# Kernel optimization log

Measured on AMD Instinct MI355X. Metric: run time of the kernel, lower is better.

Reference implementation:

```python
import jax, jax.numpy as jnp
import numpy as np


def setup_inputs() -> dict:
    key = jax.random.key(0)
    ks = jax.random.split(key, 6)
    B, Q, K = 4, 512, 1024
    Dq, Dk, Dv, H = 512, 512, 512, 128
    return {
        "queries": jax.random.normal(ks[0], (B, Q, Dq), dtype=jnp.float32),
        "keys": jax.random.normal(ks[1], (B, K, Dk), dtype=jnp.float32),
        "values": jax.random.normal(ks[2], (B, K, Dv), dtype=jnp.float32),
        "W_q": jax.random.normal(ks[3], (Dq, H), dtype=jnp.float32) / np.sqrt(Dq),
        "W_k": jax.random.normal(ks[4], (Dk, H), dtype=jnp.float32) / np.sqrt(Dk),
        "w_v": jax.random.normal(ks[5], (H,), dtype=jnp.float32) / np.sqrt(H),
    }


def reference(queries, keys, values, W_q, W_k, w_v):
    # Additive (Bahdanau) attention.
    q = jnp.einsum("bqd,dh->bqh", queries, W_q)          # [B,Q,H]
    k = jnp.einsum("bkd,dh->bkh", keys, W_k)             # [B,K,H]
    features = jnp.tanh(q[:, :, None, :] + k[:, None, :, :])  # [B,Q,K,H]
    scores = jnp.einsum("bqkh,h->bqk", features, w_v)    # [B,Q,K]
    attn = jax.nn.softmax(scores, axis=-1)               # [B,Q,K]
    return jnp.einsum("bqk,bkv->bqv", attn, values)      # [B,Q,Dv]
```

## Files before the change

kernel.cpp:

```cpp
#include <hip/hip_runtime.h>

#define BB   4
#define QS   512
#define KSZ  1024
#define DD   512
#define HH   128
#define DVV  512

typedef unsigned int uint;
typedef unsigned short ushort;
typedef unsigned long long ull;
typedef __attribute__((ext_vector_type(8)))  short short8;
typedef __attribute__((ext_vector_type(16))) float f32x16;

__device__ __forceinline__ float rcp_fast(float x)  { return __builtin_amdgcn_rcpf(x); }
__device__ __forceinline__ float exp2_fast(float x) { return __builtin_amdgcn_exp2f(x); }

__device__ __forceinline__ void split1(float v, ushort& h, ushort& l) {
    uint u = __float_as_uint(v);
    h = (ushort)(u >> 16);
    float r = v - __uint_as_float(u & 0xffff0000u);
    l = (ushort)(__float_as_uint(r) >> 16);
}

#define NSQ  (BB * QS * DD / 4 / 256)
#define NSK  (BB * KSZ * DD / 4 / 256)
#define NWT  128
#define NPJ  192
#define NVT  (BB * (KSZ / 32) * (DVV / 32))

__global__ __launch_bounds__(256) void split_kernel(
    const float* __restrict__ q, const float* __restrict__ k,
    const float* __restrict__ Wq, const float* __restrict__ Wk,
    ushort* __restrict__ qh, ushort* __restrict__ ql,
    ushort* __restrict__ kh, ushort* __restrict__ kl,
    ushort* __restrict__ wqh, ushort* __restrict__ wql,
    ushort* __restrict__ wkh, ushort* __restrict__ wkl)
{
    const int id  = blockIdx.x;
    const int tid = threadIdx.x;

    if (id < NSQ + NSK) {
        const float* src; ushort* dh; ushort* dl; size_t i;
        if (id < NSQ) { src = q; dh = qh; dl = ql; i = (size_t)id * 256 + tid; }
        else          { src = k; dh = kh; dl = kl; i = (size_t)(id - NSQ) * 256 + tid; }
        float4 v = ((const float4*)src)[i];
        ushort h0,h1,h2,h3,l0,l1,l2,l3;
        split1(v.x,h0,l0); split1(v.y,h1,l1); split1(v.z,h2,l2); split1(v.w,h3,l3);
        *(ushort4*)&dh[i * 4] = make_ushort4(h0,h1,h2,h3);
        *(ushort4*)&dl[i * 4] = make_ushort4(l0,l1,l2,l3);
        return;
    }
    __shared__ float Ts[32][33];
    int t = id - (NSQ + NSK);
    const float* W; ushort* dh; ushort* dl;
    if (t < 64) { W = Wq; dh = wqh; dl = wql; }
    else        { W = Wk; dh = wkh; dl = wkl; t -= 64; }
    const int d0 = (t >> 2) * 32, h0 = (t & 3) * 32;
    {
        const int dd = tid >> 3, c4 = (tid & 7) * 4;
        float4 v = *(const float4*)&W[(size_t)(d0 + dd) * HH + h0 + c4];
        Ts[dd][c4 + 0] = v.x; Ts[dd][c4 + 1] = v.y;
        Ts[dd][c4 + 2] = v.z; Ts[dd][c4 + 3] = v.w;
    }
    __syncthreads();
    {
        const int hh = tid >> 3, d4 = (tid & 7) * 4;
        ushort h[4], l[4];
        #pragma unroll
        for (int i = 0; i < 4; i++) split1(Ts[d4 + i][hh], h[i], l[i]);
        size_t o = (size_t)(h0 + hh) * DD + d0 + d4;
        *(ushort4*)&dh[o] = make_ushort4(h[0], h[1], h[2], h[3]);
        *(ushort4*)&dl[o] = make_ushort4(l[0], l[1], l[2], l[3]);
    }
}

__global__ __launch_bounds__(256) void projvt_kernel(
    const ushort* __restrict__ qh, const ushort* __restrict__ ql,
    const ushort* __restrict__ kh, const ushort* __restrict__ kl,
    const ushort* __restrict__ wqh, const ushort* __restrict__ wql,
    const ushort* __restrict__ wkh, const ushort* __restrict__ wkl,
    const float* __restrict__ val,
    float* __restrict__ eq, float* __restrict__ ek,
    ushort* __restrict__ vhi, ushort* __restrict__ vlo)
{
    const int id  = blockIdx.x;
    const int tid = threadIdx.x;

    if (id >= NPJ) {
        __shared__ float Ts[32][33];
        const int t   = id - NPJ;
        const int b   = t >> 9;
        const int rem = t & 511;
        const int k0  = (rem >> 4) * 32;
        const int n0  = (rem & 15) * 32;
        {
            const int kk = tid >> 3, n4 = (tid & 7) * 4;
            float4 v = *(const float4*)&val[((size_t)b * KSZ + k0 + kk) * DVV + n0 + n4];
            Ts[kk][n4 + 0] = v.x; Ts[kk][n4 + 1] = v.y;
            Ts[kk][n4 + 2] = v.z; Ts[kk][n4 + 3] = v.w;
        }
        __syncthreads();
        {
            const int nn = tid >> 3, k4 = (tid & 7) * 4;
            ushort h[4], l[4];
            #pragma unroll
            for (int i = 0; i < 4; i++) split1(Ts[k4 + i][nn], h[i], l[i]);
            size_t o = ((size_t)b * DVV + n0 + nn) * KSZ + k0 + k4;
            *(ushort4*)&vhi[o] = make_ushort4(h[0], h[1], h[2], h[3]);
            *(ushort4*)&vlo[o] = make_ushort4(l[0], l[1], l[2], l[3]);
        }
        return;
    }

    const int w = tid >> 6, lane = tid & 63;
    const int row = lane & 31, kg = lane >> 5;
    const int gw = id * 4 + w;

    const ushort *pa_h, *pa_l, *pb_h, *pb_l; float* op; int m0, nt;
    if (gw < 256) {
        m0 = (gw >> 2) * 32; nt = gw & 3;
        pa_h = qh; pa_l = ql; pb_h = wqh; pb_l = wql; op = eq;
    } else {
        const int g = gw - 256;
        m0 = (g >> 2) * 32; nt = g & 3;
        pa_h = kh; pa_l = kl; pb_h = wkh; pb_l = wkl; op = ek;
    }

    const ushort* ah_p = pa_h + (size_t)(m0 + row) * DD + kg * 8;
    const ushort* al_p = pa_l + (size_t)(m0 + row) * DD + kg * 8;
    const ushort* bh_p = pb_h + (size_t)(nt * 32 + row) * DD + kg * 8;
    const ushort* bl_p = pb_l + (size_t)(nt * 32 + row) * DD + kg * 8;

    f32x16 acc;
    #pragma unroll
    for (int i = 0; i < 16; i++) acc[i] = 0.f;

    #pragma unroll 8
    for (int ks = 0; ks < DD; ks += 16) {
        short8 ah = *(const short8*)(ah_p + ks);
        short8 al = *(const short8*)(al_p + ks);
        short8 bh = *(const short8*)(bh_p + ks);
        short8 bl = *(const short8*)(bl_p + ks);
        acc = __builtin_amdgcn_mfma_f32_32x32x16_bf16(ah, bh, acc, 0, 0, 0);
        acc = __builtin_amdgcn_mfma_f32_32x32x16_bf16(ah, bl, acc, 0, 0, 0);
        acc = __builtin_amdgcn_mfma_f32_32x32x16_bf16(al, bh, acc, 0, 0, 0);
    }

    const float C2L = 2.8853900817779268f;
    float* ob = op + (size_t)m0 * HH + nt * 32;
    #pragma unroll
    for (int r = 0; r < 16; r++) {
        const int rb = (r & 3) + 8 * (r >> 2) + 4 * kg;
        ob[(size_t)rb * HH + row] = exp2_fast(acc[r] * C2L);
    }
}

__global__ __launch_bounds__(512, 2) void spv_kernel(
    const float* __restrict__ eq, const float* __restrict__ ek,
    const float* __restrict__ wv,
    const ushort* __restrict__ vhi, const ushort* __restrict__ vlo,
    float* __restrict__ opart, float* __restrict__ rsp)
{
    __shared__ float  eqs[64][132];
    __shared__ float  eks[32][132];
    __shared__ ushort PhS[64][36];
    __shared__ ushort PlS[64][36];

    const int id  = blockIdx.x;
    const int bk  = id & 31;
    const int qt  = id >> 5;
    const int b   = bk >> 3;
    const int kp  = bk & 7;

    const int tid  = threadIdx.x;
    const int w    = tid >> 6, lane = tid & 63;
    const int col  = lane & 31, kg = lane >> 5;
    const int wq   = (w & 1) * 32;
    const int wn   = (w >> 1) * 128;
    const int tq   = tid >> 4;
    const int tk   = tid & 15;

    const float* eqg = eq + ((size_t)b * QS + qt * 64) * HH;
    #pragma unroll
    for (int i = 0; i < 4; i++) {
        int f = tid + i * 512;
        int row = f >> 5, c4 = (f & 31) * 4;
        *(float4*)&eqs[row][c4] = *(const float4*)&eqg[(size_t)row * HH + c4];
    }
    const float* ekg = ek + ((size_t)b * KSZ + kp * 128) * HH;
    #pragma unroll
    for (int i = 0; i < 2; i++) {
        int f = tid + i * 512;
        int row = f >> 5, c4 = (f & 31) * 4;
        *(float4*)&eks[row][c4] = *(const float4*)&ekg[(size_t)row * HH + c4];
    }
    __syncthreads();

    f32x16 acc[4];
    #pragma unroll
    for (int n = 0; n < 4; n++) {
        #pragma unroll
        for (int i = 0; i < 16; i++) acc[n][i] = 0.f;
    }
    float rowacc0 = 0.f, rowacc1 = 0.f;

    const size_t vrow0 = ((size_t)b * DVV + wn + col) * KSZ + kp * 128;
    const ushort* vh_p = vhi + vrow0;
    const ushort* vl_p = vlo + vrow0;

#define SGROUP(eqv, ekv, sacc) { \
    float u0 = fminf(fmaf((eqv).x, (ekv).x, 1.0f), 3e7f); \
    float u1 = fminf(fmaf((eqv).y, (ekv).y, 1.0f), 3e7f); \
    float u2 = fminf(fmaf((eqv).z, (ekv).z, 1.0f), 3e7f); \
    float u3 = fminf(fmaf((eqv).w, (ekv).w, 1.0f), 3e7f); \
    float p01 = u0 * u1, p23 = u2 * u3; \
    float n01 = fmaf(wv4.x, u1, wv4.y * u0); \
    float n23 = fmaf(wv4.z, u3, wv4.w * u2); \
    float Nn = fmaf(n01, p23, n23 * p01); \
    sacc = fmaf(Nn, rcp_fast(p01 * p23), sacc); }

    for (int s = 0; s < 4; s++) {
        uint4 bhf[8], blf[8];
        #pragma unroll
        for (int nb = 0; nb < 4; nb++) {
            #pragma unroll
            for (int k2 = 0; k2 < 2; k2++) {
                const size_t o = (size_t)(nb * 32) * KSZ + s * 32 + k2 * 16 + kg * 8;
                bhf[nb * 2 + k2] = *(const uint4*)(vh_p + o);
                blf[nb * 2 + k2] = *(const uint4*)(vl_p + o);
            }
        }
        float4 eknxt0, eknxt1;
        if (s < 3) {
            int f0 = tid, f1 = tid + 512;
            eknxt0 = *(const float4*)&ekg[(size_t)((s + 1) * 32 + (f0 >> 5)) * HH + (f0 & 31) * 4];
            eknxt1 = *(const float4*)&ekg[(size_t)((s + 1) * 32 + (f1 >> 5)) * HH + (f1 & 31) * 4];
        }

        float s00 = 0.f, s01 = 0.f, s10 = 0.f, s11 = 0.f;
        #pragma unroll 2
        for (int h = 0; h < HH; h += 4) {
            float4 wv4 = *(const float4*)&wv[h];
            float4 eqa = *(const float4*)&eqs[tq][h];
            float4 eqb = *(const float4*)&eqs[tq + 32][h];
            float4 eka = *(const float4*)&eks[tk][h];
            float4 ekb = *(const float4*)&eks[tk + 16][h];
            SGROUP(eqa, eka, s00);
            SGROUP(eqa, ekb, s01);
            SGROUP(eqb, eka, s10);
            SGROUP(eqb, ekb, s11);
        }
        {
            const float CN = -2.8853900817779268f;
            float p00 = exp2_fast(s00 * CN);
            float p01v = exp2_fast(s01 * CN);
            float p10 = exp2_fast(s10 * CN);
            float p11 = exp2_fast(s11 * CN);
            ushort hh, ll;
            split1(p00,  hh, ll); PhS[tq][tk]           = hh; PlS[tq][tk]           = ll;
            split1(p01v, hh, ll); PhS[tq][tk + 16]      = hh; PlS[tq][tk + 16]      = ll;
            split1(p10,  hh, ll); PhS[tq + 32][tk]      = hh; PlS[tq + 32][tk]      = ll;
            split1(p11,  hh, ll); PhS[tq + 32][tk + 16] = hh; PlS[tq + 32][tk + 16] = ll;
            rowacc0 += p00 + p01v;
            rowacc1 += p10 + p11;
        }
        __syncthreads();

        if (s < 3) {
            int f0 = tid, f1 = tid + 512;
            *(float4*)&eks[f0 >> 5][(f0 & 31) * 4] = eknxt0;
            *(float4*)&eks[f1 >> 5][(f1 & 31) * 4] = eknxt1;
        }

        #pragma unroll
        for (int k2 = 0; k2 < 2; k2++) {
            short8 ah, al;
            { const ull* p = (const ull*)&PhS[wq + col][k2 * 16 + kg * 8];
              ((ull*)&ah)[0] = p[0]; ((ull*)&ah)[1] = p[1]; }
            { const ull* p = (const ull*)&PlS[wq + col][k2 * 16 + kg * 8];
              ((ull*)&al)[0] = p[0]; ((ull*)&al)[1] = p[1]; }
            #pragma unroll
            for (int nb = 0; nb < 4; nb++) {
                short8 vh = *(const short8*)&bhf[nb * 2 + k2];
                short8 vl = *(const short8*)&blf[nb * 2 + k2];
                acc[nb] = __builtin_amdgcn_mfma_f32_32x32x16_bf16(ah, vh, acc[nb], 0, 0, 0);
                acc[nb] = __builtin_amdgcn_mfma_f32_32x32x16_bf16(ah, vl, acc[nb], 0, 0, 0);
                acc[nb] = __builtin_amdgcn_mfma_f32_32x32x16_bf16(al, vh, acc[nb], 0, 0, 0);
            }
        }
        __syncthreads();
    }
#undef SGROUP

    #pragma unroll
    for (int m = 8; m; m >>= 1) {
        rowacc0 += __shfl_xor(rowacc0, m);
        rowacc1 += __shfl_xor(rowacc1, m);
    }
    if (tk == 0) {
        rsp[((size_t)b * QS + qt * 64 + tq) * 8 + kp]      = rowacc0;
        rsp[((size_t)b * QS + qt * 64 + tq + 32) * 8 + kp] = rowacc1;
    }

    float* ob = opart + (((size_t)kp * BB + b) * QS + qt * 64 + wq) * DVV + wn;
    #pragma unroll
    for (int nb = 0; nb < 4; nb++) {
        #pragma unroll
        for (int r = 0; r < 16; r++) {
            const int rb = (r & 3) + 8 * (r >> 2) + 4 * kg;
            ob[(size_t)rb * DVV + nb * 32 + col] = acc[nb][r];
        }
    }
}

__global__ __launch_bounds__(256) void norm_kernel(
    const float* __restrict__ opart, const float* __restrict__ rsp,
    float* __restrict__ outp)
{
    const int i  = blockIdx.x * 256 + threadIdx.x;
    const int n4 = (i & 127) * 4;
    const int q  = (i >> 7) & (QS - 1);
    const int b  = i >> 16;

    const float* rp = rsp + ((size_t)b * QS + q) * 8;
    float4 r0 = *(const float4*)rp;
    float4 r1 = *(const float4*)(rp + 4);
    float inv = rcp_fast(r0.x + r0.y + r0.z + r0.w + r1.x + r1.y + r1.z + r1.w);

    float ox = 0.f, oy = 0.f, oz = 0.f, ow = 0.f;
    #pragma unroll
    for (int kp = 0; kp < 8; kp++) {
        float4 v = *(const float4*)&opart[(((size_t)kp * BB + b) * QS + q) * DVV + n4];
        ox += v.x; oy += v.y; oz += v.z; ow += v.w;
    }
    float4 res = make_float4(ox * inv, oy * inv, oz * inv, ow * inv);
    *(float4*)&outp[((size_t)b * QS + q) * DVV + n4] = res;
}

extern "C" void kernel_launch(void* const* d_in, const int* in_sizes, int n_in,
                              void* d_out, int out_size, void* d_ws, size_t ws_size,
                              hipStream_t stream)
{
    const float* queries = (const float*)d_in[0];
    const float* keys    = (const float*)d_in[1];
    const float* values  = (const float*)d_in[2];
    const float* Wq      = (const float*)d_in[3];
    const float* Wk      = (const float*)d_in[4];
    const float* wv      = (const float*)d_in[5];
    float* out = (float*)d_out;

    float*  eq    = (float*)d_ws;
    float*  ek    = eq  + (size_t)BB * QS * HH;
    float*  rsp   = ek  + (size_t)BB * KSZ * HH;
    float*  opart = rsp + (size_t)BB * QS * 8;
    ushort* vhi = (ushort*)(opart + (size_t)8 * BB * QS * DVV);
    ushort* vlo = vhi + (size_t)BB * KSZ * DVV;
    ushort* qh  = vlo + (size_t)BB * KSZ * DVV;
    ushort* ql  = qh  + (size_t)BB * QS * DD;
    ushort* kh  = ql  + (size_t)BB * QS * DD;
    ushort* kl  = kh  + (size_t)BB * KSZ * DD;
    ushort* wqh = kl  + (size_t)BB * KSZ * DD;
    ushort* wql = wqh + (size_t)HH * DD;
    ushort* wkh = wql + (size_t)HH * DD;
    ushort* wkl = wkh + (size_t)HH * DD;

    split_kernel<<<dim3(NSQ + NSK + NWT), 256, 0, stream>>>(
        queries, keys, Wq, Wk, qh, ql, kh, kl, wqh, wql, wkh, wkl);

    projvt_kernel<<<dim3(NPJ + NVT), 256, 0, stream>>>(
        qh, ql, kh, kl, wqh, wql, wkh, wkl, values, eq, ek, vhi, vlo);

    spv_kernel<<<dim3(256), 512, 0, stream>>>(eq, ek, wv, vhi, vlo, opart, rsp);

    norm_kernel<<<dim3(1024), 256, 0, stream>>>(opart, rsp, out);
}
```

Baseline: 152.3 us.

## Retile score-PV kernel into 16-query blocks with 16x16x32 MFMA

The fused score+PV kernel now processes 16 queries per 256-thread block instead of 64 queries per 512-thread block, launching 1024 blocks instead of 256 to fill the CUs better. The PV matmul switches from 32x32x16 to 16x16x32 bf16 MFMA with 8 accumulator tiles per wave, and each wave covers 128 output columns. The block index mapping is reordered so neighbouring blocks share the batch/key slice. The cost is that V tiles are re-read by four times as many blocks, and each block has less reuse of its staged ek tile.

```diff
diff --git a/kernel.cpp b/kernel.cpp
--- a/kernel.cpp
+++ b/kernel.cpp
@@ -12,6 +12,7 @@
 typedef unsigned long long ull;
 typedef __attribute__((ext_vector_type(8)))  short short8;
 typedef __attribute__((ext_vector_type(16))) float f32x16;
+typedef __attribute__((ext_vector_type(4)))  float f32x4;
 
 __device__ __forceinline__ float rcp_fast(float x)  { return __builtin_amdgcn_rcpf(x); }
 __device__ __forceinline__ float exp2_fast(float x) { return __builtin_amdgcn_exp2f(x); }
@@ -156,58 +157,60 @@
     }
 }
 
-__global__ __launch_bounds__(512, 2) void spv_kernel(
+__global__ __launch_bounds__(256, 4) void spv_kernel(
     const float* __restrict__ eq, const float* __restrict__ ek,
     const float* __restrict__ wv,
     const ushort* __restrict__ vhi, const ushort* __restrict__ vlo,
     float* __restrict__ opart, float* __restrict__ rsp)
 {
-    __shared__ float  eqs[64][132];
+    __shared__ float  eqs[16][132];
     __shared__ float  eks[32][132];
-    __shared__ ushort PhS[64][36];
-    __shared__ ushort PlS[64][36];
-
-    const int id  = blockIdx.x;
-    const int bk  = id & 31;
-    const int qt  = id >> 5;
-    const int b   = bk >> 3;
-    const int kp  = bk & 7;
+    __shared__ ushort PhS[16][36];
+    __shared__ ushort PlS[16][36];
+
+    const int id   = blockIdx.x;
+    const int low3 = id & 7;
+    const int rest = id >> 3;
+    const int bk   = (rest & 3) * 8 + low3;
+    const int qt   = rest >> 2;
+    const int b    = bk >> 3;
+    const int kp   = bk & 7;
 
     const int tid  = threadIdx.x;
     const int w    = tid >> 6, lane = tid & 63;
-    const int col  = lane & 31, kg = lane >> 5;
-    const int wq   = (w & 1) * 32;
-    const int wn   = (w >> 1) * 128;
     const int tq   = tid >> 4;
     const int tk   = tid & 15;
-
-    const float* eqg = eq + ((size_t)b * QS + qt * 64) * HH;
+    const int wn   = w * 128;
+    const int arow = lane & 15;
+    const int akg  = lane >> 4;
+
+    const float* eqg = eq + ((size_t)b * QS + qt * 16) * HH;
+    #pragma unroll
+    for (int i = 0; i < 2; i++) {
+        int f = tid + i * 256;
+        *(float4*)&eqs[f >> 5][(f & 31) * 4] =
+            *(const float4*)&eqg[(size_t)(f >> 5) * HH + (f & 31) * 4];
+    }
+    const float* ekg = ek + ((size_t)b * KSZ + kp * 128) * HH;
     #pragma unroll
     for (int i = 0; i < 4; i++) {
-        int f = tid + i * 512;
-        int row = f >> 5, c4 = (f & 31) * 4;
-        *(float4*)&eqs[row][c4] = *(const float4*)&eqg[(size_t)row * HH + c4];
-    }
-    const float* ekg = ek + ((size_t)b * KSZ + kp * 128) * HH;
-    #pragma unroll
-    for (int i = 0; i < 2; i++) {
-        int f = tid + i * 512;
-        int row = f >> 5, c4 = (f & 31) * 4;
-        *(float4*)&eks[row][c4] = *(const float4*)&ekg[(size_t)row * HH + c4];
+        int f = tid + i * 256;
+        *(float4*)&eks[f >> 5][(f & 31) * 4] =
+            *(const float4*)&ekg[(size_t)(f >> 5) * HH + (f & 31) * 4];
     }
     __syncthreads();
 
-    f32x16 acc[4];
-    #pragma unroll
-    for (int n = 0; n < 4; n++) {
+    f32x4 acc[8];
+    #pragma unroll
+    for (int n = 0; n < 8; n++) {
         #pragma unroll
-        for (int i = 0; i < 16; i++) acc[n][i] = 0.f;
-    }
-    float rowacc0 = 0.f, rowacc1 = 0.f;
-
-    const size_t vrow0 = ((size_t)b * DVV + wn + col) * KSZ + kp * 128;
-    const ushort* vh_p = vhi + vrow0;
-    const ushort* vl_p = vlo + vrow0;
+        for (int i = 0; i < 4; i++) acc[n][i] = 0.f;
+    }
+    float rowacc = 0.f;
+
+    const size_t vrow0 = ((size_t)b * DVV + wn + arow) * KSZ + kp * 128 + akg * 8;
+    const ushort* vhb = vhi + vrow0;
+    const ushort* vlb = vlo + vrow0;
 
 #define SGROUP(eqv, ekv, sacc) { \
     float u0 = fminf(fmaf((eqv).x, (ekv).x, 1.0f), 3e7f); \
@@ -221,96 +224,75 @@
     sacc = fmaf(Nn, rcp_fast(p01 * p23), sacc); }
 
     for (int s = 0; s < 4; s++) {
-        uint4 bhf[8], blf[8];
-        #pragma unroll
-        for (int nb = 0; nb < 4; nb++) {
+        float4 eknxt[4];
+        if (s < 3) {
             #pragma unroll
-            for (int k2 = 0; k2 < 2; k2++) {
-                const size_t o = (size_t)(nb * 32) * KSZ + s * 32 + k2 * 16 + kg * 8;
-                bhf[nb * 2 + k2] = *(const uint4*)(vh_p + o);
-                blf[nb * 2 + k2] = *(const uint4*)(vl_p + o);
+            for (int i = 0; i < 4; i++) {
+                int f = tid + i * 256;
+                eknxt[i] = *(const float4*)
+                    &ekg[(size_t)((s + 1) * 32 + (f >> 5)) * HH + (f & 31) * 4];
             }
         }
-        float4 eknxt0, eknxt1;
-        if (s < 3) {
-            int f0 = tid, f1 = tid + 512;
-            eknxt0 = *(const float4*)&ekg[(size_t)((s + 1) * 32 + (f0 >> 5)) * HH + (f0 & 31) * 4];
-            eknxt1 = *(const float4*)&ekg[(size_t)((s + 1) * 32 + (f1 >> 5)) * HH + (f1 & 31) * 4];
-        }
-
-        float s00 = 0.f, s01 = 0.f, s10 = 0.f, s11 = 0.f;
-        #pragma unroll 2
+
+        float s0 = 0.f, s1 = 0.f;
+        #pragma unroll 4
         for (int h = 0; h < HH; h += 4) {
             float4 wv4 = *(const float4*)&wv[h];
             float4 eqa = *(const float4*)&eqs[tq][h];
-            float4 eqb = *(const float4*)&eqs[tq + 32][h];
             float4 eka = *(const float4*)&eks[tk][h];
             float4 ekb = *(const float4*)&eks[tk + 16][h];
-            SGROUP(eqa, eka, s00);
-            SGROUP(eqa, ekb, s01);
-            SGROUP(eqb, eka, s10);
-            SGROUP(eqb, ekb, s11);
+            SGROUP(eqa, eka, s0);
+            SGROUP(eqa, ekb, s1);
         }
         {
             const float CN = -2.8853900817779268f;
-            float p00 = exp2_fast(s00 * CN);
-            float p01v = exp2_fast(s01 * CN);
-            float p10 = exp2_fast(s10 * CN);
-            float p11 = exp2_fast(s11 * CN);
+            float p0 = exp2_fast(s0 * CN);
+            float p1 = exp2_fast(s1 * CN);
             ushort hh, ll;
-            split1(p00,  hh, ll); PhS[tq][tk]           = hh; PlS[tq][tk]           = ll;
-            split1(p01v, hh, ll); PhS[tq][tk + 16]      = hh; PlS[tq][tk + 16]      = ll;
-            split1(p10,  hh, ll); PhS[tq + 32][tk]      = hh; PlS[tq + 32][tk]      = ll;
-            split1(p11,  hh, ll); PhS[tq + 32][tk + 16] = hh; PlS[tq + 32][tk + 16] = ll;
-            rowacc0 += p00 + p01v;
-            rowacc1 += p10 + p11;
+            split1(p0, hh, ll); PhS[tq][tk]      = hh; PlS[tq][tk]      = ll;
+            split1(p1, hh, ll); PhS[tq][tk + 16] = hh; PlS[tq][tk + 16] = ll;
+            rowacc += p0 + p1;
         }
         __syncthreads();
 
         if (s < 3) {
-            int f0 = tid, f1 = tid + 512;
-            *(float4*)&eks[f0 >> 5][(f0 & 31) * 4] = eknxt0;
-            *(float4*)&eks[f1 >> 5][(f1 & 31) * 4] = eknxt1;
-        }
-
+            #pragma unroll
+            for (int i = 0; i < 4; i++) {
+                int f = tid + i * 256;
+                *(float4*)&eks[f >> 5][(f & 31) * 4] = eknxt[i];
+            }
+        }
+
+        short8 ah, al;
+        { const ull* p = (const ull*)&PhS[arow][akg * 8];
+          ((ull*)&ah)[0] = p[0]; ((ull*)&ah)[1] = p[1]; }
+        { const ull* p = (const ull*)&PlS[arow][akg * 8];
+          ((ull*)&al)[0] = p[0]; ((ull*)&al)[1] = p[1]; }
         #pragma unroll
-        for (int k2 = 0; k2 < 2; k2++) {
-            short8 ah, al;
-            { const ull* p = (const ull*)&PhS[wq + col][k2 * 16 + kg * 8];
-              ((ull*)&ah)[0] = p[0]; ((ull*)&ah)[1] = p[1]; }
-            { const ull* p = (const ull*)&PlS[wq + col][k2 * 16 + kg * 8];
-              ((ull*)&al)[0] = p[0]; ((ull*)&al)[1] = p[1]; }
-            #pragma unroll
-            for (int nb = 0; nb < 4; nb++) {
-                short8 vh = *(const short8*)&bhf[nb * 2 + k2];
-                short8 vl = *(const short8*)&blf[nb * 2 + k2];
-                acc[nb] = __builtin_amdgcn_mfma_f32_32x32x16_bf16(ah, vh, acc[nb], 0, 0, 0);
-                acc[nb] = __builtin_amdgcn_mfma_f32_32x32x16_bf16(ah, vl, acc[nb], 0, 0, 0);
-                acc[nb] = __builtin_amdgcn_mfma_f32_32x32x16_bf16(al, vh, acc[nb], 0, 0, 0);
-            }
+        for (int nb = 0; nb < 8; nb++) {
+            const size_t o = (size_t)nb * 16 * KSZ + (size_t)s * 32;
+            short8 vh = *(const short8*)(vhb + o);
+            short8 vl = *(const short8*)(vlb + o);
+            acc[nb] = __builtin_amdgcn_mfma_f32_16x16x32_bf16(ah, vh, acc[nb], 0, 0, 0);
+            acc[nb] = __builtin_amdgcn_mfma_f32_16x16x32_bf16(ah, vl, acc[nb], 0, 0, 0);
+            acc[nb] = __builtin_amdgcn_mfma_f32_16x16x32_bf16(al, vh, acc[nb], 0, 0, 0);
         }
         __syncthreads();
     }
 #undef SGROUP
 
     #pragma unroll
-    for (int m = 8; m; m >>= 1) {
-        rowacc0 += __shfl_xor(rowacc0, m);
-        rowacc1 += __shfl_xor(rowacc1, m);
-    }
-    if (tk == 0) {
-        rsp[((size_t)b * QS + qt * 64 + tq) * 8 + kp]      = rowacc0;
-        rsp[((size_t)b * QS + qt * 64 + tq + 32) * 8 + kp] = rowacc1;
-    }
-
-    float* ob = opart + (((size_t)kp * BB + b) * QS + qt * 64 + wq) * DVV + wn;
-    #pragma unroll
-    for (int nb = 0; nb < 4; nb++) {
+    for (int m = 8; m; m >>= 1) rowacc += __shfl_xor(rowacc, m);
+    if (tk == 0)
+        rsp[((size_t)b * QS + qt * 16 + tq) * 8 + kp] = rowacc;
+
+    float* ob = opart + (((size_t)kp * BB + b) * QS + qt * 16) * DVV + wn;
+    const int orow = akg * 4;
+    #pragma unroll
+    for (int nb = 0; nb < 8; nb++) {
         #pragma unroll
-        for (int r = 0; r < 16; r++) {
-            const int rb = (r & 3) + 8 * (r >> 2) + 4 * kg;
-            ob[(size_t)rb * DVV + nb * 32 + col] = acc[nb][r];
-        }
+        for (int r = 0; r < 4; r++)
+            ob[(size_t)(orow + r) * DVV + nb * 16 + arow] = acc[nb][r];
     }
 }
 
@@ -371,7 +353,7 @@
     projvt_kernel<<<dim3(NPJ + NVT), 256, 0, stream>>>(
         qh, ql, kh, kl, wqh, wql, wkh, wkl, values, eq, ek, vhi, vlo);
 
-    spv_kernel<<<dim3(256), 512, 0, stream>>>(eq, ek, wv, vhi, vlo, opart, rsp);
+    spv_kernel<<<dim3(1024), 256, 0, stream>>>(eq, ek, wv, vhi, vlo, opart, rsp);
 
     norm_kernel<<<dim3(1024), 256, 0, stream>>>(opart, rsp, out);
 }
```

After: 158.9 us. 4.3% more time.

## Split score-PV kernel into smaller 32x64 tiles with 16-way key partitioning

Applied to the files above, without the earlier changes.

Retiles the fused score/softmax-weighted-V kernel from 256 blocks of 512 threads (64 queries x 128 keys) to 1024 blocks of 256 threads (32 queries x 64 keys), doubling the key partitions to 16. This aims to fill more compute units on the MI355X and raise occupancy. The V-fragment prefetch and ek double-buffer prefetch are replaced with loads issued directly before the MFMAs, and the extra key partitions double the partial output buffer written and then reduced by the norm kernel.

```diff
diff --git a/kernel.cpp b/kernel.cpp
--- a/kernel.cpp
+++ b/kernel.cpp
@@ -6,6 +6,7 @@
 #define DD   512
 #define HH   128
 #define DVV  512
+#define KPN  16
 
 typedef unsigned int uint;
 typedef unsigned short ushort;
@@ -156,44 +157,43 @@
     }
 }
 
-__global__ __launch_bounds__(512, 2) void spv_kernel(
+__global__ __launch_bounds__(256, 4) void spv_kernel(
     const float* __restrict__ eq, const float* __restrict__ ek,
     const float* __restrict__ wv,
     const ushort* __restrict__ vhi, const ushort* __restrict__ vlo,
     float* __restrict__ opart, float* __restrict__ rsp)
 {
-    __shared__ float  eqs[64][132];
+    __shared__ float  eqs[32][132];
     __shared__ float  eks[32][132];
-    __shared__ ushort PhS[64][36];
-    __shared__ ushort PlS[64][36];
+    __shared__ ushort PhS[32][36];
+    __shared__ ushort PlS[32][36];
 
     const int id  = blockIdx.x;
-    const int bk  = id & 31;
-    const int qt  = id >> 5;
-    const int b   = bk >> 3;
-    const int kp  = bk & 7;
+    const int kp  = id & 15;
+    const int b   = (id >> 4) & 3;
+    const int qt  = id >> 6;
 
     const int tid  = threadIdx.x;
     const int w    = tid >> 6, lane = tid & 63;
-    const int col  = lane & 31, kg = lane >> 5;
-    const int wq   = (w & 1) * 32;
-    const int wn   = (w >> 1) * 128;
     const int tq   = tid >> 4;
     const int tk   = tid & 15;
-
-    const float* eqg = eq + ((size_t)b * QS + qt * 64) * HH;
+    const int wn   = w * 128;
+    const int arow = lane & 31;
+    const int akg  = lane >> 5;
+
+    const float* eqg = eq + ((size_t)b * QS + qt * 32) * HH;
     #pragma unroll
     for (int i = 0; i < 4; i++) {
-        int f = tid + i * 512;
-        int row = f >> 5, c4 = (f & 31) * 4;
-        *(float4*)&eqs[row][c4] = *(const float4*)&eqg[(size_t)row * HH + c4];
-    }
-    const float* ekg = ek + ((size_t)b * KSZ + kp * 128) * HH;
-    #pragma unroll
-    for (int i = 0; i < 2; i++) {
-        int f = tid + i * 512;
-        int row = f >> 5, c4 = (f & 31) * 4;
-        *(float4*)&eks[row][c4] = *(const float4*)&ekg[(size_t)row * HH + c4];
+        int f = tid + i * 256;
+        *(float4*)&eqs[f >> 5][(f & 31) * 4] =
+            *(const float4*)&eqg[(size_t)(f >> 5) * HH + (f & 31) * 4];
+    }
+    const float* ekg = ek + ((size_t)b * KSZ + kp * 64) * HH;
+    #pragma unroll
+    for (int i = 0; i < 4; i++) {
+        int f = tid + i * 256;
+        *(float4*)&eks[f >> 5][(f & 31) * 4] =
+            *(const float4*)&ekg[(size_t)(f >> 5) * HH + (f & 31) * 4];
     }
     __syncthreads();
 
@@ -205,9 +205,9 @@
     }
     float rowacc0 = 0.f, rowacc1 = 0.f;
 
-    const size_t vrow0 = ((size_t)b * DVV + wn + col) * KSZ + kp * 128;
-    const ushort* vh_p = vhi + vrow0;
-    const ushort* vl_p = vlo + vrow0;
+    const size_t vrow0 = ((size_t)b * DVV + wn + arow) * KSZ + kp * 64 + akg * 8;
+    const ushort* vhb = vhi + vrow0;
+    const ushort* vlb = vlo + vrow0;
 
 #define SGROUP(eqv, ekv, sacc) { \
     float u0 = fminf(fmaf((eqv).x, (ekv).x, 1.0f), 3e7f); \
@@ -220,30 +220,14 @@
     float Nn = fmaf(n01, p23, n23 * p01); \
     sacc = fmaf(Nn, rcp_fast(p01 * p23), sacc); }
 
-    for (int s = 0; s < 4; s++) {
-        uint4 bhf[8], blf[8];
-        #pragma unroll
-        for (int nb = 0; nb < 4; nb++) {
-            #pragma unroll
-            for (int k2 = 0; k2 < 2; k2++) {
-                const size_t o = (size_t)(nb * 32) * KSZ + s * 32 + k2 * 16 + kg * 8;
-                bhf[nb * 2 + k2] = *(const uint4*)(vh_p + o);
-                blf[nb * 2 + k2] = *(const uint4*)(vl_p + o);
-            }
-        }
-        float4 eknxt0, eknxt1;
-        if (s < 3) {
-            int f0 = tid, f1 = tid + 512;
-            eknxt0 = *(const float4*)&ekg[(size_t)((s + 1) * 32 + (f0 >> 5)) * HH + (f0 & 31) * 4];
-            eknxt1 = *(const float4*)&ekg[(size_t)((s + 1) * 32 + (f1 >> 5)) * HH + (f1 & 31) * 4];
-        }
-
+    #pragma unroll
+    for (int s = 0; s < 2; s++) {
         float s00 = 0.f, s01 = 0.f, s10 = 0.f, s11 = 0.f;
-        #pragma unroll 2
+        #pragma unroll 4
         for (int h = 0; h < HH; h += 4) {
             float4 wv4 = *(const float4*)&wv[h];
             float4 eqa = *(const float4*)&eqs[tq][h];
-            float4 eqb = *(const float4*)&eqs[tq + 32][h];
+            float4 eqb = *(const float4*)&eqs[tq + 16][h];
             float4 eka = *(const float4*)&eks[tk][h];
             float4 ekb = *(const float4*)&eks[tk + 16][h];
             SGROUP(eqa, eka, s00);
@@ -260,34 +244,44 @@
             ushort hh, ll;
             split1(p00,  hh, ll); PhS[tq][tk]           = hh; PlS[tq][tk]           = ll;
             split1(p01v, hh, ll); PhS[tq][tk + 16]      = hh; PlS[tq][tk + 16]      = ll;
-            split1(p10,  hh, ll); PhS[tq + 32][tk]      = hh; PlS[tq + 32][tk]      = ll;
-            split1(p11,  hh, ll); PhS[tq + 32][tk + 16] = hh; PlS[tq + 32][tk + 16] = ll;
+            split1(p10,  hh, ll); PhS[tq + 16][tk]      = hh; PlS[tq + 16][tk]      = ll;
+            split1(p11,  hh, ll); PhS[tq + 16][tk + 16] = hh; PlS[tq + 16][tk + 16] = ll;
             rowacc0 += p00 + p01v;
             rowacc1 += p10 + p11;
         }
         __syncthreads();
 
-        if (s < 3) {
-            int f0 = tid, f1 = tid + 512;
-            *(float4*)&eks[f0 >> 5][(f0 & 31) * 4] = eknxt0;
-            *(float4*)&eks[f1 >> 5][(f1 & 31) * 4] = eknxt1;
-        }
-
+        if (s == 0) {
+            #pragma unroll
+            for (int i = 0; i < 4; i++) {
+                int f = tid + i * 256;
+                *(float4*)&eks[f >> 5][(f & 31) * 4] =
+                    *(const float4*)&ekg[(size_t)(32 + (f >> 5)) * HH + (f & 31) * 4];
+            }
+        }
+
+        short8 ah0, al0, ah1, al1;
+        { const ull* p = (const ull*)&PhS[arow][akg * 8];
+          ((ull*)&ah0)[0] = p[0]; ((ull*)&ah0)[1] = p[1]; }
+        { const ull* p = (const ull*)&PlS[arow][akg * 8];
+          ((ull*)&al0)[0] = p[0]; ((ull*)&al0)[1] = p[1]; }
+        { const ull* p = (const ull*)&PhS[arow][16 + akg * 8];
+          ((ull*)&ah1)[0] = p[0]; ((ull*)&ah1)[1] = p[1]; }
+        { const ull* p = (const ull*)&PlS[arow][16 + akg * 8];
+          ((ull*)&al1)[0] = p[0]; ((ull*)&al1)[1] = p[1]; }
         #pragma unroll
-        for (int k2 = 0; k2 < 2; k2++) {
-            short8 ah, al;
-            { const ull* p = (const ull*)&PhS[wq + col][k2 * 16 + kg * 8];
-              ((ull*)&ah)[0] = p[0]; ((ull*)&ah)[1] = p[1]; }
-            { const ull* p = (const ull*)&PlS[wq + col][k2 * 16 + kg * 8];
-              ((ull*)&al)[0] = p[0]; ((ull*)&al)[1] = p[1]; }
-            #pragma unroll
-            for (int nb = 0; nb < 4; nb++) {
-                short8 vh = *(const short8*)&bhf[nb * 2 + k2];
-                short8 vl = *(const short8*)&blf[nb * 2 + k2];
-                acc[nb] = __builtin_amdgcn_mfma_f32_32x32x16_bf16(ah, vh, acc[nb], 0, 0, 0);
-                acc[nb] = __builtin_amdgcn_mfma_f32_32x32x16_bf16(ah, vl, acc[nb], 0, 0, 0);
-                acc[nb] = __builtin_amdgcn_mfma_f32_32x32x16_bf16(al, vh, acc[nb], 0, 0, 0);
-            }
+        for (int nb = 0; nb < 4; nb++) {
+            const size_t o = (size_t)nb * 32 * KSZ + (size_t)s * 32;
+            short8 vh0 = *(const short8*)(vhb + o);
+            short8 vl0 = *(const short8*)(vlb + o);
+            short8 vh1 = *(const short8*)(vhb + o + 16);
+            short8 vl1 = *(const short8*)(vlb + o + 16);
+            acc[nb] = __builtin_amdgcn_mfma_f32_32x32x16_bf16(ah0, vh0, acc[nb], 0, 0, 0);
+            acc[nb] = __builtin_amdgcn_mfma_f32_32x32x16_bf16(ah0, vl0, acc[nb], 0, 0, 0);
+            acc[nb] = __builtin_amdgcn_mfma_f32_32x32x16_bf16(al0, vh0, acc[nb], 0, 0, 0);
+            acc[nb] = __builtin_amdgcn_mfma_f32_32x32x16_bf16(ah1, vh1, acc[nb], 0, 0, 0);
+            acc[nb] = __builtin_amdgcn_mfma_f32_32x32x16_bf16(ah1, vl1, acc[nb], 0, 0, 0);
+            acc[nb] = __builtin_amdgcn_mfma_f32_32x32x16_bf16(al1, vh1, acc[nb], 0, 0, 0);
         }
         __syncthreads();
     }
@@ -299,17 +293,17 @@
         rowacc1 += __shfl_xor(rowacc1, m);
     }
     if (tk == 0) {
-        rsp[((size_t)b * QS + qt * 64 + tq) * 8 + kp]      = rowacc0;
-        rsp[((size_t)b * QS + qt * 64 + tq + 32) * 8 + kp] = rowacc1;
-    }
-
-    float* ob = opart + (((size_t)kp * BB + b) * QS + qt * 64 + wq) * DVV + wn;
+        rsp[((size_t)b * QS + qt * 32 + tq) * KPN + kp]      = rowacc0;
+        rsp[((size_t)b * QS + qt * 32 + tq + 16) * KPN + kp] = rowacc1;
+    }
+
+    float* ob = opart + (((size_t)kp * BB + b) * QS + qt * 32) * DVV + wn;
     #pragma unroll
     for (int nb = 0; nb < 4; nb++) {
         #pragma unroll
         for (int r = 0; r < 16; r++) {
-            const int rb = (r & 3) + 8 * (r >> 2) + 4 * kg;
-            ob[(size_t)rb * DVV + nb * 32 + col] = acc[nb][r];
+            const int rb = (r & 3) + 8 * (r >> 2) + 4 * akg;
+            ob[(size_t)rb * DVV + nb * 32 + arow] = acc[nb][r];
         }
     }
 }
@@ -323,14 +317,18 @@
     const int q  = (i >> 7) & (QS - 1);
     const int b  = i >> 16;
 
-    const float* rp = rsp + ((size_t)b * QS + q) * 8;
-    float4 r0 = *(const float4*)rp;
-    float4 r1 = *(const float4*)(rp + 4);
-    float inv = rcp_fast(r0.x + r0.y + r0.z + r0.w + r1.x + r1.y + r1.z + r1.w);
+    const float* rp = rsp + ((size_t)b * QS + q) * KPN;
+    float s = 0.f;
+    #pragma unroll
+    for (int j = 0; j < KPN / 4; j++) {
+        float4 r = *(const float4*)(rp + j * 4);
+        s += r.x + r.y + r.z + r.w;
+    }
+    float inv = rcp_fast(s);
 
     float ox = 0.f, oy = 0.f, oz = 0.f, ow = 0.f;
     #pragma unroll
-    for (int kp = 0; kp < 8; kp++) {
+    for (int kp = 0; kp < KPN; kp++) {
         float4 v = *(const float4*)&opart[(((size_t)kp * BB + b) * QS + q) * DVV + n4];
         ox += v.x; oy += v.y; oz += v.z; ow += v.w;
     }
@@ -353,8 +351,8 @@
     float*  eq    = (float*)d_ws;
     float*  ek    = eq  + (size_t)BB * QS * HH;
     float*  rsp   = ek  + (size_t)BB * KSZ * HH;
-    float*  opart = rsp + (size_t)BB * QS * 8;
-    ushort* vhi = (ushort*)(opart + (size_t)8 * BB * QS * DVV);
+    float*  opart = rsp + (size_t)BB * QS * KPN;
+    ushort* vhi = (ushort*)(opart + (size_t)KPN * BB * QS * DVV);
     ushort* vlo = vhi + (size_t)BB * KSZ * DVV;
     ushort* qh  = vlo + (size_t)BB * KSZ * DVV;
     ushort* ql  = qh  + (size_t)BB * QS * DD;
@@ -371,7 +369,7 @@
     projvt_kernel<<<dim3(NPJ + NVT), 256, 0, stream>>>(
         qh, ql, kh, kl, wqh, wql, wkh, wkl, values, eq, ek, vhi, vlo);
 
-    spv_kernel<<<dim3(256), 512, 0, stream>>>(eq, ek, wv, vhi, vlo, opart, rsp);
+    spv_kernel<<<dim3(1024), 256, 0, stream>>>(eq, ek, wv, vhi, vlo, opart, rsp);
 
     norm_kernel<<<dim3(1024), 256, 0, stream>>>(opart, rsp, out);
 }
```

Result: no change. 153.6 us (+0.9%).
